# Optimization experiments

Measured on AMD Instinct MI355X. Metric: run time of the kernel, lower is better.

## Reference

```python
import jax, jax.numpy as jnp
import numpy as np

B_, L_, DM, DI, N, R, K = 2, 1024, 1024, 2048, 16, 64, 4
EPS = 1e-5

def silu(x):
    return x * jax.nn.sigmoid(x)

def causal_conv1d(x, w, b):
    # x: (B,L,D); w: (D,K) depthwise. torch Conv1d(padding=K-1) then slice [:L] == left-pad causal conv.
    L = x.shape[1]
    xp = jnp.pad(x, ((0, 0), (K - 1, 0), (0, 0)))
    y = xp[:, 0:L, :] * w[:, 0]
    for k in range(1, K):
        y = y + xp[:, k:k + L, :] * w[:, k]
    return y + b

def selective_scan(u, delta, A, Bm, Cm, D):
    # u, delta: (B,L,D); A: (D,N); Bm, Cm: (B,L,N)
    dA = jnp.exp(jnp.einsum('bld,dn->bldn', delta, A))
    dBu = jnp.einsum('bld,bln,bld->bldn', delta, Bm, u)
    h0 = jnp.zeros((u.shape[0], u.shape[2], A.shape[1]), u.dtype)
    def step(h, xs):
        dA_t, dBu_t, C_t = xs
        h = dA_t * h + dBu_t
        return h, jnp.einsum('bdn,bn->bd', h, C_t)
    _, ys = jax.lax.scan(step, h0, (jnp.moveaxis(dA, 1, 0), jnp.moveaxis(dBu, 1, 0), jnp.moveaxis(Cm, 1, 0)))
    return jnp.moveaxis(ys, 0, 1) + u * D  # (B,L,D)

def branch(x, conv_w, conv_b, Wx, Wdt, bdt, A_log, D):
    x = silu(causal_conv1d(x, conv_w, conv_b))
    dbl = x @ Wx.T                               # (B,L,R+2N)
    dt, Bm, Cm = dbl[..., :R], dbl[..., R:R + N], dbl[..., R + N:]
    dt = dt @ Wdt.T + bdt                        # dt_proj is Linear WITH bias in source
    delta = jax.nn.softplus(dt + bdt)            # source also passes delta_bias to the scan (bias added twice; faithful)
    A = -jnp.exp(A_log)
    return selective_scan(x, delta, A, Bm, Cm, D)

def reference(a, b, Wi, conv_w, conv_b, Wx, Wdt, bdt, A_log, D,
              conv_w_b, conv_b_b, Wx_b, Wdt_b, bdt_b, A_log_b, D_b, Wo, norm_w):
    xz_a = a @ Wi.T
    x_f, z = xz_a[..., :DI], xz_a[..., DI:]
    y_f = branch(x_f, conv_w, conv_b, Wx, Wdt, bdt, A_log, D)
    xz_b = jnp.flip(b, 1) @ Wi.T
    x_bwd = xz_b[..., :DI]
    y_b = jnp.flip(branch(x_bwd, conv_w_b, conv_b_b, Wx_b, Wdt_b, bdt_b, A_log_b, D_b), 1)
    y = y_f + y_b
    # RMSNormGated, norm_before_gate=False: gate first, then RMSNorm
    g = y * silu(z)
    g = g * jax.lax.rsqrt(jnp.mean(g * g, axis=-1, keepdims=True) + EPS) * norm_w
    return g @ Wo.T

def setup_inputs() -> dict:
    key = jax.random.key(0)
    ks = jax.random.split(key, 16)
    s = 0.02
    def rn(k, shape):
        return jax.random.normal(k, shape, jnp.float32) * s
    def inv_dt(k):
        dt = jnp.exp(jax.random.uniform(k, (DI,)) * (np.log(0.1) - np.log(0.001)) + np.log(0.001))
        dt = jnp.clip(dt, 1e-4, None)
        return dt + jnp.log(-jnp.expm1(-dt))
    A_log = jnp.log(jnp.broadcast_to(jnp.arange(1, N + 1, dtype=jnp.float32), (DI, N)))
    return dict(
        a=jax.random.normal(ks[0], (B_, L_, DM), jnp.float32),
        b=jax.random.normal(ks[1], (B_, L_, DM), jnp.float32),
        Wi=rn(ks[2], (2 * DI, DM)),
        conv_w=rn(ks[3], (DI, K)), conv_b=rn(ks[4], (DI,)),
        Wx=rn(ks[5], (R + 2 * N, DI)), Wdt=rn(ks[6], (DI, R)), bdt=inv_dt(ks[7]),
        A_log=A_log, D=jnp.ones((DI,), jnp.float32),
        conv_w_b=rn(ks[8], (DI, K)), conv_b_b=rn(ks[9], (DI,)),
        Wx_b=rn(ks[10], (R + 2 * N, DI)), Wdt_b=rn(ks[11], (DI, R)), bdt_b=inv_dt(ks[12]),
        A_log_b=A_log, D_b=jnp.ones((DI,), jnp.float32),
        Wo=rn(ks[13], (DM, DI)), norm_w=jnp.ones((DI,), jnp.float32),
    )
```

## Files before the change

### kernel.cpp

```cpp
#include <hip/hip_runtime.h>
#include <hip/hip_bf16.h>
#include <cmath>

#define B_ 2
#define L_ 1024
#define DM 1024
#define DI 2048
#define NS 16
#define RR 64
#define KC 4
#define NCH 64
#define CL (L_ / NCH)
#define NSPLIT 16

using frag8 = __attribute__((ext_vector_type(8))) short;
using facc4 = __attribute__((ext_vector_type(4))) float;
using f32x4 = __attribute__((ext_vector_type(4))) float;

struct alignas(8) S4v { short x, y, z, w; };

__device__ __forceinline__ short f2b(float v) {
    __hip_bfloat16 h = __float2bfloat16(v);
    return *(short*)&h;
}

__device__ __forceinline__ float silu1(float x) {
    return x / (1.f + __expf(-x));
}

__device__ __forceinline__ int swz(int r, int q) {
    return (r * 4 + (q ^ (r & 3))) ^ (((r >> 2) & 1) << 2);
}
__device__ __forceinline__ void swz_src(int l, int& R, int& C) {
    int rho = l >> 2;
    R = rho ^ ((rho >> 2) & 1);
    C = (l & 3) ^ (R & 3);
}

__device__ __forceinline__ void pow4(float qv, f32x4& p0, f32x4& p1, f32x4& p2, f32x4& p3) {
    float q2 = qv * qv, q3 = q2 * qv, q4 = q2 * q2;
    p0 = (f32x4){qv, q2, q3, q4};
    f32x4 s4 = {q4, q4, q4, q4};
    p1 = p0 * s4;
    f32x4 s8 = s4 * s4;
    p2 = p0 * s8;
    p3 = p1 * s8;
}

__device__ __forceinline__ void async_ld16(const void* g, void* l) {
    __builtin_amdgcn_global_load_lds(
        (const __attribute__((address_space(1))) unsigned int*)g,
        (__attribute__((address_space(3))) unsigned int*)l, 16, 0, 0);
}

__device__ __forceinline__ void cvt4(const float* __restrict__ src, size_t si,
                                     short* __restrict__ dst, size_t di2) {
    float4 v = *(const float4*)(src + si);
    S4v r = { f2b(v.x), f2b(v.y), f2b(v.z), f2b(v.w) };
    *(S4v*)(dst + di2) = r;
}

__global__ void cvt_all(const float* __restrict__ a, const float* __restrict__ b,
                        const float* __restrict__ Wi,
                        const float* __restrict__ Wx, const float* __restrict__ Wxb2,
                        const float* __restrict__ Wdt, const float* __restrict__ Wdtb2,
                        const float* __restrict__ Wo,
                        short* __restrict__ abf, short* __restrict__ bbf,
                        short* __restrict__ Wibf,
                        short* __restrict__ Wxbf, short* __restrict__ Wxbbf,
                        short* __restrict__ Wdtbf, short* __restrict__ Wdtbbf,
                        short* __restrict__ Wobf) {
    size_t i = ((size_t)blockIdx.x * 256 + threadIdx.x) * 4;
    const size_t S_ab = (size_t)B_ * L_ * DM;
    if (i < S_ab) { cvt4(a, i, abf, i); return; } i -= S_ab;
    if (i < S_ab) {
        size_t r = i / DM, c = i % DM;
        size_t bb = r / L_, ll = r % L_;
        size_t sr = bb * L_ + (L_ - 1 - ll);
        cvt4(b, sr * DM + c, bbf, i); return;
    } i -= S_ab;
    const size_t S_wi = (size_t)2 * DI * DM;
    if (i < S_wi) { cvt4(Wi, i, Wibf, i); return; } i -= S_wi;
    const size_t S_wx = (size_t)96 * DI;
    if (i < S_wx) { cvt4(Wx, i, Wxbf, i); return; } i -= S_wx;
    if (i < S_wx) { cvt4(Wxb2, i, Wxbbf, i); return; } i -= S_wx;
    const size_t S_wd = (size_t)DI * RR;
    if (i < S_wd) { cvt4(Wdt, i, Wdtbf, i); return; } i -= S_wd;
    if (i < S_wd) { cvt4(Wdtb2, i, Wdtbbf, i); return; } i -= S_wd;
    const size_t S_wo = (size_t)DM * DI;
    if (i < S_wo) cvt4(Wo, i, Wobf, i);
}

template <int BM>
__device__ __forceinline__ void gemm_body(
    const short* A, int lda, const short* W, int ldw, int wRowOff,
    float* C, int ldc, int K, int m0, int n0) {
    constexpr int MF = BM / 32;
    __shared__ __align__(16) short As[2][BM * 32];
    __shared__ __align__(16) short Ws[2][64 * 32];
    const int tid = threadIdx.x;
    const int lane = tid & 63, wv = tid >> 6;
    const int wm = (wv & 1) * (BM / 2), wn = (wv >> 1) * 32;
    const int q = lane >> 4, mr = lane & 15;
    int sR, sC; swz_src(lane, sR, sC);
    const int sg = swz(mr, q) * 8;

    const short* Ag = A + (size_t)(m0 + wv * 16 + sR) * lda + sC * 8;
    const short* Wg = W + (size_t)(n0 + wRowOff + wv * 16 + sR) * ldw + sC * 8;

    facc4 acc[MF][2];
#pragma unroll
    for (int i = 0; i < MF; ++i)
#pragma unroll
        for (int j = 0; j < 2; ++j) acc[i][j] = (facc4){0.f, 0.f, 0.f, 0.f};

    async_ld16(Ag, &As[0][wv * 512]);
    if constexpr (BM == 128) async_ld16(Ag + (size_t)64 * lda, &As[0][wv * 512 + 2048]);
    async_ld16(Wg, &Ws[0][wv * 512]);

    const int nk = K / 32;
    for (int it = 0; it < nk; ++it) {
        const int buf = it & 1;
        __syncthreads();
        if (it + 1 < nk) {
            int k0 = (it + 1) * 32;
            async_ld16(Ag + k0, &As[buf ^ 1][wv * 512]);
            if constexpr (BM == 128)
                async_ld16(Ag + (size_t)64 * lda + k0, &As[buf ^ 1][wv * 512 + 2048]);
            async_ld16(Wg + k0, &Ws[buf ^ 1][wv * 512]);
        }
        frag8 af[MF], wf[2];
#pragma unroll
        for (int t = 0; t < MF; ++t)
            af[t] = *(const frag8*)&As[buf][(wm + t * 16) * 32 + sg];
#pragma unroll
        for (int j = 0; j < 2; ++j)
            wf[j] = *(const frag8*)&Ws[buf][(wn + j * 16) * 32 + sg];
#pragma unroll
        for (int i = 0; i < MF; ++i)
#pragma unroll
            for (int j = 0; j < 2; ++j)
                acc[i][j] = __builtin_amdgcn_mfma_f32_16x16x32_bf16(af[i], wf[j], acc[i][j], 0, 0, 0);
    }
#pragma unroll
    for (int i = 0; i < MF; ++i)
#pragma unroll
        for (int j = 0; j < 2; ++j) {
            int gn = n0 + wn + j * 16 + mr;
#pragma unroll
            for (int e = 0; e < 4; ++e) {
                int gm = m0 + wm + i * 16 + q * 4 + e;
                C[(size_t)gm * ldc + gn] = acc[i][j][e];
            }
        }
}

__global__ __launch_bounds__(256) void gemm_xz_conv(
    const short* __restrict__ abf, const short* __restrict__ bbf,
    const short* __restrict__ Wibf,
    float* __restrict__ UF, float* __restrict__ UB, float* __restrict__ Z,
    short* __restrict__ CFo, short* __restrict__ CBo,
    const float* __restrict__ cwf, const float* __restrict__ cbf2,
    const float* __restrict__ cwb, const float* __restrict__ cbb2) {
    __shared__ __align__(16) char smem[26624];
    short (*As)[4608] = (short (*)[4608])smem;
    short (*Ws)[2048] = (short (*)[2048])(smem + 18432);
    float (*Xs)[68] = (float (*)[68])smem;

    const int bz = blockIdx.z;
    const bool isX = (bz != 2);
    const int tid = threadIdx.x;
    const int lane = tid & 63, wv = tid >> 6;
    {
    }
    const int id = blockIdx.y * gridDim.x + blockIdx.x;
    const int xcd = id & 7, idx = id >> 3;
    const int nt = (xcd & 3) * 8 + (idx & 7);
    const int mt = (xcd >> 2) * 8 + (idx >> 3);
    const int m0 = mt * 128, n0 = nt * 64;
    const bool hasHalo = isX && (m0 % L_ != 0);
    const int wm = (wv & 1) * 64, wn = (wv >> 1) * 32;
    const int q = lane >> 4, mr = lane & 15;
    int sR, sC; swz_src(lane, sR, sC);
    const int sg = swz(mr, q) * 8;

    const short* A = (bz == 1) ? bbf : abf;
    const int wOff = (bz == 2) ? DI : 0;

    const short* Ag  = A + (size_t)(m0 + wv * 16 + sR) * DM + sC * 8;
    const short* Agh = A + (size_t)(m0 - 16 + sR) * DM + sC * 8;
    const short* Wg  = Wibf + (size_t)(n0 + wOff + wv * 16 + sR) * DM + sC * 8;

    facc4 acc[4][2], hacc[2];
#pragma unroll
    for (int i = 0; i < 4; ++i)
#pragma unroll
        for (int j = 0; j < 2; ++j) acc[i][j] = (facc4){0.f, 0.f, 0.f, 0.f};
#pragma unroll
    for (int j = 0; j < 2; ++j) hacc[j] = (facc4){0.f, 0.f, 0.f, 0.f};

    async_ld16(Ag, &As[0][wv * 512]);
    async_ld16(Ag + (size_t)64 * DM, &As[0][wv * 512 + 2048]);
    async_ld16(Wg, &Ws[0][wv * 512]);
    if (hasHalo && wv == 0) async_ld16(Agh, &As[0][4096]);

    const int nk = DM / 32;
    for (int it = 0; it < nk; ++it) {
        const int buf = it & 1;
        __syncthreads();
        if (it + 1 < nk) {
            int k0 = (it + 1) * 32;
            async_ld16(Ag + k0, &As[buf ^ 1][wv * 512]);
            async_ld16(Ag + (size_t)64 * DM + k0, &As[buf ^ 1][wv * 512 + 2048]);
            async_ld16(Wg + k0, &Ws[buf ^ 1][wv * 512]);
            if (hasHalo && wv == 0) async_ld16(Agh + k0, &As[buf ^ 1][4096]);
        }
        frag8 af[4], wf[2];
#pragma unroll
        for (int t = 0; t < 4; ++t)
            af[t] = *(const frag8*)&As[buf][(wm + t * 16) * 32 + sg];
#pragma unroll
        for (int j = 0; j < 2; ++j)
            wf[j] = *(const frag8*)&Ws[buf][(wn + j * 16) * 32 + sg];
        if (hasHalo && wm == 0) {
            frag8 afh = *(const frag8*)&As[buf][4096 + sg];
#pragma unroll
            for (int j = 0; j < 2; ++j)
                hacc[j] = __builtin_amdgcn_mfma_f32_16x16x32_bf16(afh, wf[j], hacc[j], 0, 0, 0);
        }
#pragma unroll
        for (int i = 0; i < 4; ++i)
#pragma unroll
            for (int j = 0; j < 2; ++j)
                acc[i][j] = __builtin_amdgcn_mfma_f32_16x16x32_bf16(af[i], wf[j], acc[i][j], 0, 0, 0);
    }

    if (!isX) {
#pragma unroll
        for (int i = 0; i < 4; ++i)
#pragma unroll
            for (int j = 0; j < 2; ++j) {
                int gn = n0 + wn + j * 16 + mr;
#pragma unroll
                for (int e = 0; e < 4; ++e) {
                    int gm = m0 + wm + i * 16 + q * 4 + e;
                    Z[(size_t)gm * DI + gn] = acc[i][j][e];
                }
            }
        return;
    }

    const float* cw = (bz == 1) ? cwb : cwf;
    const float* cb = (bz == 1) ? cbb2 : cbf2;
    float* U   = (bz == 1) ? UB : UF;
    short* Co  = (bz == 1) ? CBo : CFo;
    const int col = tid & 63;
    const int dcol = n0 + col;
    const int rg = tid >> 6;
    float4 wd = *(const float4*)(cw + (size_t)dcol * KC);
    float bd = cb[dcol];

    __syncthreads();
#pragma unroll
    for (int p = 0; p < 2; ++p) {
        if (p == 0) {
            if ((wv & 1) == 0) {
#pragma unroll
                for (int j = 0; j < 2; ++j) {
#pragma unroll
                    for (int e = 0; e < 4; ++e)
                        Xs[q * 4 + e][wn + j * 16 + mr] = hacc[j][e];
#pragma unroll
                    for (int i = 0; i < 4; ++i)
#pragma unroll
                        for (int e = 0; e < 4; ++e)
                            Xs[16 + i * 16 + q * 4 + e][wn + j * 16 + mr] = acc[i][j][e];
                }
            }
        } else {
            if ((wv & 1) == 0) {
#pragma unroll
                for (int j = 0; j < 2; ++j)
#pragma unroll
                    for (int e = 0; e < 4; ++e)
                        Xs[q * 4 + e][wn + j * 16 + mr] = acc[3][j][e];
            } else {
#pragma unroll
                for (int j = 0; j < 2; ++j)
#pragma unroll
                    for (int i = 0; i < 4; ++i)
#pragma unroll
                        for (int e = 0; e < 4; ++e)
                            Xs[16 + i * 16 + q * 4 + e][wn + j * 16 + mr] = acc[i][j][e];
            }
        }
        __syncthreads();
#pragma unroll
        for (int rr = 0; rr < 16; ++rr) {
            int rl = rg * 16 + rr;
            float x0 = Xs[13 + rl][col];
            float x1 = Xs[14 + rl][col];
            float x2 = Xs[15 + rl][col];
            float x3 = Xs[16 + rl][col];
            float v = bd + x0 * wd.x + x1 * wd.y + x2 * wd.z + x3 * wd.w;
            float s2 = silu1(v);
            size_t go = (size_t)(m0 + p * 64 + rl) * DI + dcol;
            U[go] = s2;
            Co[go] = f2b(s2);
        }
        if (p == 0) __syncthreads();
    }
}

__global__ __launch_bounds__(256) void gemm_dt(
    const short* __restrict__ dtf, const short* __restrict__ dtb,
    const short* __restrict__ Wf, const short* __restrict__ Wb,
    float* __restrict__ DTF_, float* __restrict__ DTB_) {
    const int bz = blockIdx.z;
    gemm_body<64>(bz ? dtb : dtf, RR, bz ? Wb : Wf, RR, 0,
                  bz ? DTB_ : DTF_, DI, RR, blockIdx.y * 64, blockIdx.x * 64);
}

__global__ __launch_bounds__(256) void gemm_out(
    const short* __restrict__ gbf, const short* __restrict__ Wobf,
    float* __restrict__ out) {
    gemm_body<64>(gbf, DI, Wobf, DI, 0, out, DM, DI, blockIdx.y * 64, blockIdx.x * 64);
}

__global__ __launch_bounds__(256) void gemm_dbl(
    const short* __restrict__ CF, const short* __restrict__ CB,
    const short* __restrict__ Wxf, const short* __restrict__ Wxb,
    float* __restrict__ part) {
    __shared__ __align__(16) short As[2][128 * 32];
    __shared__ __align__(16) short Ws[2][96 * 32];
    const int br = blockIdx.z / NSPLIT, zz = blockIdx.z % NSPLIT;
    const short* A = br ? CB : CF;
    const short* W = br ? Wxb : Wxf;
    constexpr int Kchunk = DI / NSPLIT;
    const int tid = threadIdx.x;
    const int lane = tid & 63, wv = tid >> 6;
    const int m0 = blockIdx.y * 128;
    const int kOff = zz * Kchunk;
    const int wm = (wv & 1) * 64, wn = (wv >> 1) * 48;
    const int q = lane >> 4, mr = lane & 15;
    int sR, sC; swz_src(lane, sR, sC);
    const int sg = swz(mr, q) * 8;

    const short* Ag = A + (size_t)(m0 + wv * 16 + sR) * DI + sC * 8 + kOff;
    const short* Wg = W + (size_t)(wv * 16 + sR) * DI + sC * 8 + kOff;

    facc4 acc[4][3];
#pragma unroll
    for (int i = 0; i < 4; ++i)
#pragma unroll
        for (int j = 0; j < 3; ++j) acc[i][j] = (facc4){0.f, 0.f, 0.f, 0.f};

    async_ld16(Ag, &As[0][wv * 512]);
    async_ld16(Ag + (size_t)64 * DI, &As[0][wv * 512 + 2048]);
    async_ld16(Wg, &Ws[0][wv * 512]);
    if (wv < 2) async_ld16(Wg + (size_t)64 * DI, &Ws[0][wv * 512 + 2048]);

    const int nk = Kchunk / 32;
    for (int it = 0; it < nk; ++it) {
        const int buf = it & 1;
        __syncthreads();
        if (it + 1 < nk) {
            int k0 = (it + 1) * 32;
            async_ld16(Ag + k0, &As[buf ^ 1][wv * 512]);
            async_ld16(Ag + (size_t)64 * DI + k0, &As[buf ^ 1][wv * 512 + 2048]);
            async_ld16(Wg + k0, &Ws[buf ^ 1][wv * 512]);
            if (wv < 2) async_ld16(Wg + (size_t)64 * DI + k0, &Ws[buf ^ 1][wv * 512 + 2048]);
        }
        frag8 af[4], wf[3];
#pragma unroll
        for (int t = 0; t < 4; ++t)
            af[t] = *(const frag8*)&As[buf][(wm + t * 16) * 32 + sg];
#pragma unroll
        for (int j = 0; j < 3; ++j)
            wf[j] = *(const frag8*)&Ws[buf][(wn + j * 16) * 32 + sg];
#pragma unroll
        for (int i = 0; i < 4; ++i)
#pragma unroll
            for (int j = 0; j < 3; ++j)
                acc[i][j] = __builtin_amdgcn_mfma_f32_16x16x32_bf16(af[i], wf[j], acc[i][j], 0, 0, 0);
    }
    float* Cz = part + (size_t)blockIdx.z * (B_ * L_) * 96;
#pragma unroll
    for (int i = 0; i < 4; ++i)
#pragma unroll
        for (int j = 0; j < 3; ++j) {
            int gn = wn + j * 16 + mr;
#pragma unroll
            for (int e = 0; e < 4; ++e) {
                int gm = m0 + wm + i * 16 + q * 4 + e;
                Cz[(size_t)gm * 96 + gn] = acc[i][j][e];
            }
        }
}

__global__ void reduce_dbl(const float* __restrict__ part,
                           float* __restrict__ dblf, float* __restrict__ dblb,
                           short* __restrict__ dtf, short* __restrict__ dtb) {
    int idx = blockIdx.x * blockDim.x + threadIdx.x;
    const int T = B_ * L_ * 96;
    int br = 0;
    if (idx >= T) { br = 1; idx -= T; }
    const float* p = part + (size_t)br * NSPLIT * T;
    float s = 0.f;
#pragma unroll
    for (int z = 0; z < NSPLIT; ++z) s += p[(size_t)z * T + idx];
    (br ? dblb : dblf)[idx] = s;
    int row = idx / 96, col = idx % 96;
    if (col < RR) (br ? dtb : dtf)[(size_t)row * RR + col] = f2b(s);
}

__device__ __forceinline__ float softplus2(float raw, float bd2) {
    float x = raw + bd2;
    return (x > 20.f) ? x : log1pf(__expf(x));
}

__global__ void scan_chunk(float* UF, float* UB, float* DTFm, float* DTBm,
                           const float* bdtf, const float* bdtb,
                           const float* dblF, const float* dblB,
                           const float* Alf, const float* Alb,
                           const float* Dvf, const float* Dvb,
                           float* PF, float* SF, float* PB, float* SB) {
    __shared__ __align__(16) float BCs[CL][32];
    const int tid = threadIdx.x;
    const int d = blockIdx.x * 256 + tid;
    const int br = blockIdx.y >> 1, bb = blockIdx.y & 1;
    const int c = blockIdx.z;
    const int l0 = c * CL;
    float* __restrict__ u = br ? UB : UF;
    float* __restrict__ dtm = br ? DTBm : DTFm;
    const float* __restrict__ bdt = br ? bdtb : bdtf;
    const float* __restrict__ dbl = br ? dblB : dblF;
    const float* __restrict__ A_log = br ? Alb : Alf;
    const float* __restrict__ Dv = br ? Dvb : Dvf;
    float* __restrict__ Pbuf = br ? PB : PF;
    float* __restrict__ Sbuf = br ? SB : SF;
    {
        int e = tid * 2;
        int row = e >> 5, cc = e & 31;
        *(float2*)&BCs[row][cc] =
            *(const float2*)(dbl + ((size_t)(bb * L_ + l0 + row) * 96 + 64 + cc));
    }
    float Av[NS];
#pragma unroll
    for (int n = 0; n < NS; ++n) Av[n] = -__expf(A_log[d * NS + n]);
    bool structured = true;
#pragma unroll
    for (int n = 1; n < NS; ++n)
        structured = structured &&
            (fabsf(Av[n] - (n + 1) * Av[0]) <= 1e-4f * (n + 1) * fabsf(Av[0]));
    const float bd2 = 2.f * bdt[d];
    const float Dd = Dv[d];
    float cd = 0.f;
    __syncthreads();
    float* __restrict__ up = u + ((size_t)bb * L_ + l0) * DI + d;
    float* __restrict__ dp = dtm + ((size_t)bb * L_ + l0) * DI + d;
    size_t pb = ((size_t)(bb * NCH + c) * NS) * DI + d;

    if (structured) {
        const float Av0 = Av[0];
        f32x4 S4[4];
#pragma unroll
        for (int m = 0; m < 4; ++m) S4[m] = (f32x4){0.f, 0.f, 0.f, 0.f};
        float draw = dp[0], ul = up[0];
        for (int l = 0; l < CL; ++l) {
            float draw_n = 0.f, ul_n = 0.f;
            if (l + 1 < CL) { draw_n = dp[(size_t)(l + 1) * DI]; ul_n = up[(size_t)(l + 1) * DI]; }
            float x = draw + bd2;
            float e = __expf(x);
            float del = (x > 20.f) ? x : __logf(1.f + e);
            cd += del;
            float du = del * ul;
            f32x4 pw0, pw1, pw2, pw3;
            pow4(__expf(del * Av0), pw0, pw1, pw2, pw3);
            const f32x4* BC4 = (const f32x4*)&BCs[l][0];
            f32x4 b0 = BC4[0], b1 = BC4[1], b2 = BC4[2], b3 = BC4[3];
            f32x4 c0 = BC4[4], c1 = BC4[5], c2 = BC4[6], c3 = BC4[7];
            f32x4 du4 = {du, du, du, du};
            S4[0] = pw0 * S4[0] + du4 * b0;
            S4[1] = pw1 * S4[1] + du4 * b1;
            S4[2] = pw2 * S4[2] + du4 * b2;
            S4[3] = pw3 * S4[3] + du4 * b3;
            f32x4 pA = S4[0] * c0 + S4[1] * c1;
            f32x4 pB = S4[2] * c2 + S4[3] * c3;
            f32x4 pv = pA + pB;
            float accv = (pv[0] + pv[1]) + (pv[2] + pv[3]);
            dp[(size_t)l * DI] = cd;
            up[(size_t)l * DI] = accv + ul * Dd;
            draw = draw_n; ul = ul_n;
        }
        f32x4 pw0, pw1, pw2, pw3;
        pow4(__expf(cd * Av0), pw0, pw1, pw2, pw3);
        f32x4 pws[4] = {pw0, pw1, pw2, pw3};
#pragma unroll
        for (int m = 0; m < 4; ++m)
#pragma unroll
            for (int k2 = 0; k2 < 4; ++k2) {
                Pbuf[pb + (size_t)(m * 4 + k2) * DI] = pws[m][k2];
                Sbuf[pb + (size_t)(m * 4 + k2) * DI] = S4[m][k2];
            }
    } else {
        float S[NS];
#pragma unroll
        for (int n = 0; n < NS; ++n) S[n] = 0.f;
        float draw = dp[0], ul = up[0];
        for (int l = 0; l < CL; ++l) {
            float draw_n = 0.f, ul_n = 0.f;
            if (l + 1 < CL) { draw_n = dp[(size_t)(l + 1) * DI]; ul_n = up[(size_t)(l + 1) * DI]; }
            float del = softplus2(draw, bd2);
            cd += del;
            float du = del * ul;
            const float* Brow = &BCs[l][0];
            float pa[4] = {0.f, 0.f, 0.f, 0.f};
#pragma unroll
            for (int j = 0; j < 4; ++j)
#pragma unroll
                for (int k = 0; k < 4; ++k) {
                    int n = j * 4 + k;
                    float dA = __expf(del * Av[n]);
                    S[n] = fmaf(dA, S[n], du * Brow[n]);
                    pa[j] = fmaf(S[n], Brow[16 + n], pa[j]);
                }
            float accv = (pa[0] + pa[1]) + (pa[2] + pa[3]);
            dp[(size_t)l * DI] = cd;
            up[(size_t)l * DI] = accv + ul * Dd;
            draw = draw_n; ul = ul_n;
        }
#pragma unroll
        for (int n = 0; n < NS; ++n) {
            Pbuf[pb + (size_t)n * DI] = __expf(cd * Av[n]);
            Sbuf[pb + (size_t)n * DI] = S[n];
        }
    }
}

__global__ void scan_combine(float* __restrict__ PF, const float* __restrict__ SF,
                             float* __restrict__ PB, const float* __restrict__ SB) {
    int g = blockIdx.x * blockDim.x + threadIdx.x;
    const int T = B_ * NS * DI;
    float* __restrict__ P = (g < T) ? PF : PB;
    const float* __restrict__ S = (g < T) ? SF : SB;
    int gg = (g < T) ? g : g - T;
    int d = gg % DI;
    int rest = gg / DI;
    int n = rest % NS, bb = rest / NS;
    const size_t stride = (size_t)NS * DI;
    size_t o = ((size_t)(bb * NCH) * NS + n) * DI + d;
    float h = 0.f;
    float Pc[4], Sc[4], Pn[4], Sn[4];
#pragma unroll
    for (int i = 0; i < 4; ++i) { Pc[i] = P[o + (size_t)i * stride]; Sc[i] = S[o + (size_t)i * stride]; }
    for (int c = 0; c < NCH; c += 4) {
        if (c + 4 < NCH) {
#pragma unroll
            for (int i = 0; i < 4; ++i) {
                Pn[i] = P[o + (size_t)(i + 4) * stride];
                Sn[i] = S[o + (size_t)(i + 4) * stride];
            }
        }
#pragma unroll
        for (int i = 0; i < 4; ++i) {
            P[o] = h;
            h = fmaf(Pc[i], h, Sc[i]);
            o += stride;
        }
#pragma unroll
        for (int i = 0; i < 4; ++i) { Pc[i] = Pn[i]; Sc[i] = Sn[i]; }
    }
}

__global__ void scan_apply(float* UF, float* UB,
                           const float* DTFm, const float* DTBm,
                           const float* dblF, const float* dblB,
                           const float* Alf, const float* Alb,
                           const float* PF, const float* PB) {
    __shared__ __align__(16) float Cs[CL][16];
    const int tid = threadIdx.x;
    const int d = blockIdx.x * 256 + tid;
    const int br = blockIdx.y >> 1, bb = blockIdx.y & 1;
    const int c = blockIdx.z + 1;
    const int l0 = c * CL;
    float* __restrict__ y = br ? UB : UF;
    const float* __restrict__ cdm = br ? DTBm : DTFm;
    const float* __restrict__ dbl = br ? dblB : dblF;
    const float* __restrict__ A_log = br ? Alb : Alf;
    const float* __restrict__ Hbuf = br ? PB : PF;
    {
        int row = tid >> 4, cc = tid & 15;
        Cs[row][cc] = dbl[(size_t)(bb * L_ + l0 + row) * 96 + 80 + cc];
    }
    float Av[NS];
#pragma unroll
    for (int n = 0; n < NS; ++n) Av[n] = -__expf(A_log[d * NS + n]);
    bool structured = true;
#pragma unroll
    for (int n = 1; n < NS; ++n)
        structured = structured &&
            (fabsf(Av[n] - (n + 1) * Av[0]) <= 1e-4f * (n + 1) * fabsf(Av[0]));
    size_t pb = ((size_t)(bb * NCH + c) * NS) * DI + d;
    const float* __restrict__ cp = cdm + ((size_t)bb * L_ + l0) * DI + d;
    float* __restrict__ yp = y + ((size_t)bb * L_ + l0) * DI + d;

    if (structured) {
        f32x4 ch4[4];
#pragma unroll
        for (int m = 0; m < 4; ++m)
#pragma unroll
            for (int k2 = 0; k2 < 4; ++k2)
                ch4[m][k2] = Hbuf[pb + (size_t)(m * 4 + k2) * DI];
        __syncthreads();
        const float Av0 = Av[0];
        float cdv = cp[0], yv = yp[0];
        for (int l = 0; l < CL; ++l) {
            float cdn = 0.f, yn = 0.f;
            if (l + 1 < CL) { cdn = cp[(size_t)(l + 1) * DI]; yn = yp[(size_t)(l + 1) * DI]; }
            f32x4 pw0, pw1, pw2, pw3;
            pow4(__expf(cdv * Av0), pw0, pw1, pw2, pw3);
            const f32x4* C4 = (const f32x4*)&Cs[l][0];
            f32x4 pA = pw0 * (C4[0] * ch4[0]) + pw1 * (C4[1] * ch4[1]);
            f32x4 pB = pw2 * (C4[2] * ch4[2]) + pw3 * (C4[3] * ch4[3]);
            f32x4 pv = pA + pB;
            yp[(size_t)l * DI] = yv + (pv[0] + pv[1]) + (pv[2] + pv[3]);
            cdv = cdn; yv = yn;
        }
    } else {
        float chs[NS];
#pragma unroll
        for (int n = 0; n < NS; ++n) chs[n] = Hbuf[pb + (size_t)n * DI];
        __syncthreads();
        float cdv = cp[0], yv = yp[0];
        for (int l = 0; l < CL; ++l) {
            float cdn = 0.f, yn = 0.f;
            if (l + 1 < CL) { cdn = cp[(size_t)(l + 1) * DI]; yn = yp[(size_t)(l + 1) * DI]; }
            const float* Crow = &Cs[l][0];
            float pa[4] = {0.f, 0.f, 0.f, 0.f};
#pragma unroll
            for (int j = 0; j < 4; ++j)
#pragma unroll
                for (int k = 0; k < 4; ++k) {
                    int n = j * 4 + k;
                    pa[j] = fmaf(__expf(cdv * Av[n]), Crow[n] * chs[n], pa[j]);
                }
            yp[(size_t)l * DI] = yv + (pa[0] + pa[1]) + (pa[2] + pa[3]);
            cdv = cdn; yv = yn;
        }
    }
}

__global__ void combine_rms(const float* __restrict__ yf, const float* __restrict__ yb,
                            const float* __restrict__ z,
                            const float* __restrict__ nw,
                            short* __restrict__ g) {
    int row = blockIdx.x;
    int bb = row / L_, l = row % L_;
    int tid = threadIdx.x;
    size_t base = (size_t)row * DI;
    size_t baseb = ((size_t)bb * L_ + (L_ - 1 - l)) * DI;
    float4 gv[2];
    float ss = 0.f;
#pragma unroll
    for (int j = 0; j < 2; ++j) {
        int d = tid * 4 + j * 1024;
        float4 a4 = *(const float4*)(yf + base + d);
        float4 b4 = *(const float4*)(yb + baseb + d);
        float4 z4 = *(const float4*)(z + base + d);
        float4 r;
        r.x = (a4.x + b4.x) * silu1(z4.x);
        r.y = (a4.y + b4.y) * silu1(z4.y);
        r.z = (a4.z + b4.z) * silu1(z4.z);
        r.w = (a4.w + b4.w) * silu1(z4.w);
        gv[j] = r;
        ss += r.x * r.x + r.y * r.y + r.z * r.z + r.w * r.w;
    }
#pragma unroll
    for (int off = 32; off > 0; off >>= 1) ss += __shfl_down(ss, off, 64);
    __shared__ float red[4];
    if ((tid & 63) == 0) red[tid >> 6] = ss;
    __syncthreads();
    float tot = red[0] + red[1] + red[2] + red[3];
    float rms = rsqrtf(tot / (float)DI + 1e-5f);
#pragma unroll
    for (int j = 0; j < 2; ++j) {
        int d = tid * 4 + j * 1024;
        float4 w4 = *(const float4*)(nw + d);
        S4v o = { f2b(gv[j].x * rms * w4.x), f2b(gv[j].y * rms * w4.y),
                  f2b(gv[j].z * rms * w4.z), f2b(gv[j].w * rms * w4.w) };
        *(S4v*)(g + base + d) = o;
    }
}

extern "C" void kernel_launch(void* const* d_in, const int* in_sizes, int n_in,
                              void* d_out, int out_size, void* d_ws, size_t ws_size,
                              hipStream_t stream) {
    const float* a      = (const float*)d_in[0];
    const float* b      = (const float*)d_in[1];
    const float* Wi     = (const float*)d_in[2];
    const float* conv_w = (const float*)d_in[3];
    const float* conv_b = (const float*)d_in[4];
    const float* Wx     = (const float*)d_in[5];
    const float* Wdt    = (const float*)d_in[6];
    const float* bdt    = (const float*)d_in[7];
    const float* A_log  = (const float*)d_in[8];
    const float* Dvec   = (const float*)d_in[9];
    const float* conv_w_b = (const float*)d_in[10];
    const float* conv_b_b = (const float*)d_in[11];
    const float* Wx_b   = (const float*)d_in[12];
    const float* Wdt_b  = (const float*)d_in[13];
    const float* bdt_b  = (const float*)d_in[14];
    const float* A_log_b = (const float*)d_in[15];
    const float* Dvec_b = (const float*)d_in[16];
    const float* Wo     = (const float*)d_in[17];
    const float* nw     = (const float*)d_in[18];
    float* out = (float*)d_out;

    const int M = B_ * L_;
    const size_t BLD = (size_t)M * DI;
    const size_t NDBL = (size_t)M * 96;
    const size_t PSsz = (size_t)NCH * B_ * NS * DI;

    float* f = (float*)d_ws;
    float* Zb   = f;  f += BLD;
    float* UF   = f;  f += BLD;
    float* UB   = f;  f += BLD;
    float* DTF  = f;  f += BLD;
    float* DTB  = f;  f += BLD;
    float* dblf = f;  f += NDBL;
    float* dblb = f;  f += NDBL;
    float* Pf   = f;  f += PSsz;
    float* Sf   = f;  f += PSsz;
    float* Pb   = f;  f += PSsz;
    float* Sb   = f;  f += PSsz;
    float* part = Pf;

    short* s = (short*)f;
    short* abf    = s;  s += (size_t)M * DM;
    short* bbf    = s;  s += (size_t)M * DM;
    short* Wibf   = s;  s += (size_t)2 * DI * DM;
    short* CF     = s;  s += BLD;
    short* CB     = s;  s += BLD;
    short* Wxbf   = s;  s += (size_t)96 * DI;
    short* Wxbbf  = s;  s += (size_t)96 * DI;
    short* Wdtbf  = s;  s += (size_t)DI * RR;
    short* Wdtbbf = s;  s += (size_t)DI * RR;
    short* dtfbf  = s;  s += (size_t)M * RR;
    short* dtbbf  = s;  s += (size_t)M * RR;
    short* Wobf   = s;  s += (size_t)DM * DI;
    short* gbf    = abf;

    dim3 blk(256);

    cvt_all<<<dim3(10880), blk, 0, stream>>>(a, b, Wi, Wx, Wx_b, Wdt, Wdt_b, Wo,
                                             abf, bbf, Wibf, Wxbf, Wxbbf, Wdtbf, Wdtbbf, Wobf);
    gemm_xz_conv<<<dim3(DI / 64, M / 128, 3), blk, 0, stream>>>(
        abf, bbf, Wibf, UF, UB, Zb, CF, CB,
        conv_w, conv_b, conv_w_b, conv_b_b);
    gemm_dbl<<<dim3(1, M / 128, 2 * NSPLIT), blk, 0, stream>>>(CF, CB, Wxbf, Wxbbf, part);
    reduce_dbl<<<dim3(2 * (int)(NDBL / 256)), blk, 0, stream>>>(part, dblf, dblb, dtfbf, dtbbf);
    gemm_dt<<<dim3(DI / 64, M / 64, 2), blk, 0, stream>>>(dtfbf, dtbbf, Wdtbf, Wdtbbf, DTF, DTB);
    scan_chunk<<<dim3(DI / 256, 4, NCH), blk, 0, stream>>>(
        UF, UB, DTF, DTB, bdt, bdt_b, dblf, dblb, A_log, A_log_b, Dvec, Dvec_b,
        Pf, Sf, Pb, Sb);
    scan_combine<<<dim3(2 * B_ * NS * DI / 256), blk, 0, stream>>>(Pf, Sf, Pb, Sb);
    scan_apply<<<dim3(DI / 256, 4, NCH - 1), blk, 0, stream>>>(
        UF, UB, DTF, DTB, dblf, dblb, A_log, A_log_b, Pf, Pb);
    combine_rms<<<dim3(M), blk, 0, stream>>>(UF, UB, Zb, nw, gbf);
    gemm_out<<<dim3(DM / 64, M / 64), blk, 0, stream>>>(gbf, Wobf, out);
}
```

Measured before the change: 294.8 us.

## Fuse x and z input projections per block and recompute chunk decay in combine

```diff
diff --git a/kernel.cpp b/kernel.cpp
--- a/kernel.cpp
+++ b/kernel.cpp
@@ -11,7 +11,7 @@
 #define KC 4
 #define NCH 64
 #define CL (L_ / NCH)
-#define NSPLIT 16
+#define NSPLIT 8
 
 using frag8 = __attribute__((ext_vector_type(8))) short;
 using facc4 = __attribute__((ext_vector_type(4))) float;
@@ -162,46 +162,49 @@
     short* __restrict__ CFo, short* __restrict__ CBo,
     const float* __restrict__ cwf, const float* __restrict__ cbf2,
     const float* __restrict__ cwb, const float* __restrict__ cbb2) {
-    __shared__ __align__(16) char smem[26624];
-    short (*As)[4608] = (short (*)[4608])smem;
-    short (*Ws)[2048] = (short (*)[2048])(smem + 18432);
+    __shared__ __align__(16) char smem[34816];
+    short (*As)[4608]  = (short (*)[4608])smem;
+    short (*Wsx)[2048] = (short (*)[2048])(smem + 18432);
+    short (*Wsz)[2048] = (short (*)[2048])(smem + 26624);
     float (*Xs)[68] = (float (*)[68])smem;
 
     const int bz = blockIdx.z;
-    const bool isX = (bz != 2);
+    const bool hasZ = (bz == 0);
     const int tid = threadIdx.x;
     const int lane = tid & 63, wv = tid >> 6;
-    {
-    }
     const int id = blockIdx.y * gridDim.x + blockIdx.x;
     const int xcd = id & 7, idx = id >> 3;
     const int nt = (xcd & 3) * 8 + (idx & 7);
     const int mt = (xcd >> 2) * 8 + (idx >> 3);
     const int m0 = mt * 128, n0 = nt * 64;
-    const bool hasHalo = isX && (m0 % L_ != 0);
+    const bool hasHalo = (m0 % L_ != 0);
     const int wm = (wv & 1) * 64, wn = (wv >> 1) * 32;
     const int q = lane >> 4, mr = lane & 15;
     int sR, sC; swz_src(lane, sR, sC);
     const int sg = swz(mr, q) * 8;
 
-    const short* A = (bz == 1) ? bbf : abf;
-    const int wOff = (bz == 2) ? DI : 0;
+    const short* A = bz ? bbf : abf;
 
     const short* Ag  = A + (size_t)(m0 + wv * 16 + sR) * DM + sC * 8;
     const short* Agh = A + (size_t)(m0 - 16 + sR) * DM + sC * 8;
-    const short* Wg  = Wibf + (size_t)(n0 + wOff + wv * 16 + sR) * DM + sC * 8;
-
-    facc4 acc[4][2], hacc[2];
+    const short* Wgx = Wibf + (size_t)(n0 + wv * 16 + sR) * DM + sC * 8;
+    const short* Wgz = Wibf + (size_t)(n0 + DI + wv * 16 + sR) * DM + sC * 8;
+
+    facc4 accx[4][2], accz[4][2], hacc[2];
 #pragma unroll
     for (int i = 0; i < 4; ++i)
 #pragma unroll
-        for (int j = 0; j < 2; ++j) acc[i][j] = (facc4){0.f, 0.f, 0.f, 0.f};
+        for (int j = 0; j < 2; ++j) {
+            accx[i][j] = (facc4){0.f, 0.f, 0.f, 0.f};
+            accz[i][j] = (facc4){0.f, 0.f, 0.f, 0.f};
+        }
 #pragma unroll
     for (int j = 0; j < 2; ++j) hacc[j] = (facc4){0.f, 0.f, 0.f, 0.f};
 
     async_ld16(Ag, &As[0][wv * 512]);
     async_ld16(Ag + (size_t)64 * DM, &As[0][wv * 512 + 2048]);
-    async_ld16(Wg, &Ws[0][wv * 512]);
+    async_ld16(Wgx, &Wsx[0][wv * 512]);
+    if (hasZ) async_ld16(Wgz, &Wsz[0][wv * 512]);
     if (hasHalo && wv == 0) async_ld16(Agh, &As[0][4096]);
 
     const int nk = DM / 32;
@@ -212,30 +215,43 @@
             int k0 = (it + 1) * 32;
             async_ld16(Ag + k0, &As[buf ^ 1][wv * 512]);
             async_ld16(Ag + (size_t)64 * DM + k0, &As[buf ^ 1][wv * 512 + 2048]);
-            async_ld16(Wg + k0, &Ws[buf ^ 1][wv * 512]);
+            async_ld16(Wgx + k0, &Wsx[buf ^ 1][wv * 512]);
+            if (hasZ) async_ld16(Wgz + k0, &Wsz[buf ^ 1][wv * 512]);
             if (hasHalo && wv == 0) async_ld16(Agh + k0, &As[buf ^ 1][4096]);
         }
-        frag8 af[4], wf[2];
+        frag8 af[4], wfx[2], wfz[2];
 #pragma unroll
         for (int t = 0; t < 4; ++t)
             af[t] = *(const frag8*)&As[buf][(wm + t * 16) * 32 + sg];
 #pragma unroll
         for (int j = 0; j < 2; ++j)
-            wf[j] = *(const frag8*)&Ws[buf][(wn + j * 16) * 32 + sg];
+            wfx[j] = *(const frag8*)&Wsx[buf][(wn + j * 16) * 32 + sg];
+        if (hasZ) {
+#pragma unroll
+            for (int j = 0; j < 2; ++j)
+                wfz[j] = *(const frag8*)&Wsz[buf][(wn + j * 16) * 32 + sg];
+        }
         if (hasHalo && wm == 0) {
             frag8 afh = *(const frag8*)&As[buf][4096 + sg];
 #pragma unroll
             for (int j = 0; j < 2; ++j)
-                hacc[j] = __builtin_amdgcn_mfma_f32_16x16x32_bf16(afh, wf[j], hacc[j], 0, 0, 0);
+                hacc[j] = __builtin_amdgcn_mfma_f32_16x16x32_bf16(afh, wfx[j], hacc[j], 0, 0, 0);
         }
 #pragma unroll
         for (int i = 0; i < 4; ++i)
 #pragma unroll
             for (int j = 0; j < 2; ++j)
-                acc[i][j] = __builtin_amdgcn_mfma_f32_16x16x32_bf16(af[i], wf[j], acc[i][j], 0, 0, 0);
-    }
-
-    if (!isX) {
+                accx[i][j] = __builtin_amdgcn_mfma_f32_16x16x32_bf16(af[i], wfx[j], accx[i][j], 0, 0, 0);
+        if (hasZ) {
+#pragma unroll
+            for (int i = 0; i < 4; ++i)
+#pragma unroll
+                for (int j = 0; j < 2; ++j)
+                    accz[i][j] = __builtin_amdgcn_mfma_f32_16x16x32_bf16(af[i], wfz[j], accz[i][j], 0, 0, 0);
+        }
+    }
+
+    if (hasZ) {
 #pragma unroll
         for (int i = 0; i < 4; ++i)
 #pragma unroll
@@ -244,16 +260,15 @@
 #pragma unroll
                 for (int e = 0; e < 4; ++e) {
                     int gm = m0 + wm + i * 16 + q * 4 + e;
-                    Z[(size_t)gm * DI + gn] = acc[i][j][e];
+                    Z[(size_t)gm * DI + gn] = accz[i][j][e];
                 }
             }
-        return;
-    }
-
-    const float* cw = (bz == 1) ? cwb : cwf;
-    const float* cb = (bz == 1) ? cbb2 : cbf2;
-    float* U   = (bz == 1) ? UB : UF;
-    short* Co  = (bz == 1) ? CBo : CFo;
+    }
+
+    const float* cw = bz ? cwb : cwf;
+    const float* cb = bz ? cbb2 : cbf2;
+    float* U   = bz ? UB : UF;
+    short* Co  = bz ? CBo : CFo;
     const int col = tid & 63;
     const int dcol = n0 + col;
     const int rg = tid >> 6;
@@ -274,7 +289,7 @@
                     for (int i = 0; i < 4; ++i)
 #pragma unroll
                         for (int e = 0; e < 4; ++e)
-                            Xs[16 + i * 16 + q * 4 + e][wn + j * 16 + mr] = acc[i][j][e];
+                            Xs[16 + i * 16 + q * 4 + e][wn + j * 16 + mr] = accx[i][j][e];
                 }
             }
         } else {
@@ -283,7 +298,7 @@
                 for (int j = 0; j < 2; ++j)
 #pragma unroll
                     for (int e = 0; e < 4; ++e)
-                        Xs[q * 4 + e][wn + j * 16 + mr] = acc[3][j][e];
+                        Xs[q * 4 + e][wn + j * 16 + mr] = accx[3][j][e];
             } else {
 #pragma unroll
                 for (int j = 0; j < 2; ++j)
@@ -291,7 +306,7 @@
                     for (int i = 0; i < 4; ++i)
 #pragma unroll
                         for (int e = 0; e < 4; ++e)
-                            Xs[16 + i * 16 + q * 4 + e][wn + j * 16 + mr] = acc[i][j][e];
+                            Xs[16 + i * 16 + q * 4 + e][wn + j * 16 + mr] = accx[i][j][e];
             }
         }
         __syncthreads();
@@ -317,8 +332,8 @@
     const short* __restrict__ Wf, const short* __restrict__ Wb,
     float* __restrict__ DTF_, float* __restrict__ DTB_) {
     const int bz = blockIdx.z;
-    gemm_body<64>(bz ? dtb : dtf, RR, bz ? Wb : Wf, RR, 0,
-                  bz ? DTB_ : DTF_, DI, RR, blockIdx.y * 64, blockIdx.x * 64);
+    gemm_body<128>(bz ? dtb : dtf, RR, bz ? Wb : Wf, RR, 0,
+                   bz ? DTB_ : DTF_, DI, RR, blockIdx.y * 128, blockIdx.x * 64);
 }
 
 __global__ __launch_bounds__(256) void gemm_out(
@@ -424,7 +439,7 @@
                            const float* dblF, const float* dblB,
                            const float* Alf, const float* Alb,
                            const float* Dvf, const float* Dvb,
-                           float* PF, float* SF, float* PB, float* SB) {
+                           float* SF, float* SB) {
     __shared__ __align__(16) float BCs[CL][32];
     const int tid = threadIdx.x;
     const int d = blockIdx.x * 256 + tid;
@@ -437,7 +452,6 @@
     const float* __restrict__ dbl = br ? dblB : dblF;
     const float* __restrict__ A_log = br ? Alb : Alf;
     const float* __restrict__ Dv = br ? Dvb : Dvf;
-    float* __restrict__ Pbuf = br ? PB : PF;
     float* __restrict__ Sbuf = br ? SB : SF;
     {
         int e = tid * 2;
@@ -493,16 +507,11 @@
             up[(size_t)l * DI] = accv + ul * Dd;
             draw = draw_n; ul = ul_n;
         }
-        f32x4 pw0, pw1, pw2, pw3;
-        pow4(__expf(cd * Av0), pw0, pw1, pw2, pw3);
-        f32x4 pws[4] = {pw0, pw1, pw2, pw3};
 #pragma unroll
         for (int m = 0; m < 4; ++m)
 #pragma unroll
-            for (int k2 = 0; k2 < 4; ++k2) {
-                Pbuf[pb + (size_t)(m * 4 + k2) * DI] = pws[m][k2];
+            for (int k2 = 0; k2 < 4; ++k2)
                 Sbuf[pb + (size_t)(m * 4 + k2) * DI] = S4[m][k2];
-            }
     } else {
         float S[NS];
 #pragma unroll
@@ -531,45 +540,54 @@
             draw = draw_n; ul = ul_n;
         }
 #pragma unroll
-        for (int n = 0; n < NS; ++n) {
-            Pbuf[pb + (size_t)n * DI] = __expf(cd * Av[n]);
+        for (int n = 0; n < NS; ++n)
             Sbuf[pb + (size_t)n * DI] = S[n];
-        }
     }
 }
 
 __global__ void scan_combine(float* __restrict__ PF, const float* __restrict__ SF,
-                             float* __restrict__ PB, const float* __restrict__ SB) {
+                             float* __restrict__ PB, const float* __restrict__ SB,
+                             const float* __restrict__ DTFm, const float* __restrict__ DTBm,
+                             const float* __restrict__ Alf, const float* __restrict__ Alb) {
     int g = blockIdx.x * blockDim.x + threadIdx.x;
     const int T = B_ * NS * DI;
-    float* __restrict__ P = (g < T) ? PF : PB;
-    const float* __restrict__ S = (g < T) ? SF : SB;
-    int gg = (g < T) ? g : g - T;
+    int br = (g >= T);
+    int gg = br ? g - T : g;
+    float* __restrict__ P = br ? PB : PF;
+    const float* __restrict__ S = br ? SB : SF;
+    const float* __restrict__ cdm = br ? DTBm : DTFm;
+    const float* __restrict__ Alog = br ? Alb : Alf;
     int d = gg % DI;
     int rest = gg / DI;
     int n = rest % NS, bb = rest / NS;
+    const float Avn = -__expf(Alog[d * NS + n]);
     const size_t stride = (size_t)NS * DI;
+    const size_t cstride = (size_t)CL * DI;
     size_t o = ((size_t)(bb * NCH) * NS + n) * DI + d;
+    const float* cp = cdm + ((size_t)bb * L_ + CL - 1) * DI + d;
     float h = 0.f;
-    float Pc[4], Sc[4], Pn[4], Sn[4];
-#pragma unroll
-    for (int i = 0; i < 4; ++i) { Pc[i] = P[o + (size_t)i * stride]; Sc[i] = S[o + (size_t)i * stride]; }
+    float Cc[4], Sc[4], Cn[4], Sn[4];
+#pragma unroll
+    for (int i = 0; i < 4; ++i) {
+        Cc[i] = cp[(size_t)i * cstride];
+        Sc[i] = S[o + (size_t)i * stride];
+    }
     for (int c = 0; c < NCH; c += 4) {
         if (c + 4 < NCH) {
 #pragma unroll
             for (int i = 0; i < 4; ++i) {
-                Pn[i] = P[o + (size_t)(i + 4) * stride];
+                Cn[i] = cp[(size_t)(c + i + 4) * cstride];
                 Sn[i] = S[o + (size_t)(i + 4) * stride];
             }
         }
 #pragma unroll
         for (int i = 0; i < 4; ++i) {
             P[o] = h;
-            h = fmaf(Pc[i], h, Sc[i]);
+            h = fmaf(__expf(Cc[i] * Avn), h, Sc[i]);
             o += stride;
         }
 #pragma unroll
-        for (int i = 0; i < 4; ++i) { Pc[i] = Pn[i]; Sc[i] = Sn[i]; }
+        for (int i = 0; i < 4; ++i) { Cc[i] = Cn[i]; Sc[i] = Sn[i]; }
     }
 }
 
@@ -755,16 +773,17 @@
 
     cvt_all<<<dim3(10880), blk, 0, stream>>>(a, b, Wi, Wx, Wx_b, Wdt, Wdt_b, Wo,
                                              abf, bbf, Wibf, Wxbf, Wxbbf, Wdtbf, Wdtbbf, Wobf);
-    gemm_xz_conv<<<dim3(DI / 64, M / 128, 3), blk, 0, stream>>>(
+    gemm_xz_conv<<<dim3(DI / 64, M / 128, 2), blk, 0, stream>>>(
         abf, bbf, Wibf, UF, UB, Zb, CF, CB,
         conv_w, conv_b, conv_w_b, conv_b_b);
     gemm_dbl<<<dim3(1, M / 128, 2 * NSPLIT), blk, 0, stream>>>(CF, CB, Wxbf, Wxbbf, part);
     reduce_dbl<<<dim3(2 * (int)(NDBL / 256)), blk, 0, stream>>>(part, dblf, dblb, dtfbf, dtbbf);
-    gemm_dt<<<dim3(DI / 64, M / 64, 2), blk, 0, stream>>>(dtfbf, dtbbf, Wdtbf, Wdtbbf, DTF, DTB);
+    gemm_dt<<<dim3(DI / 64, M / 128, 2), blk, 0, stream>>>(dtfbf, dtbbf, Wdtbf, Wdtbbf, DTF, DTB);
     scan_chunk<<<dim3(DI / 256, 4, NCH), blk, 0, stream>>>(
         UF, UB, DTF, DTB, bdt, bdt_b, dblf, dblb, A_log, A_log_b, Dvec, Dvec_b,
-        Pf, Sf, Pb, Sb);
-    scan_combine<<<dim3(2 * B_ * NS * DI / 256), blk, 0, stream>>>(Pf, Sf, Pb, Sb);
+        Sf, Sb);
+    scan_combine<<<dim3(2 * B_ * NS * DI / 256), blk, 0, stream>>>(
+        Pf, Sf, Pb, Sb, DTF, DTB, A_log, A_log_b);
     scan_apply<<<dim3(DI / 256, 4, NCH - 1), blk, 0, stream>>>(
         UF, UB, DTF, DTB, dblf, dblb, A_log, A_log_b, Pf, Pb);
     combine_rms<<<dim3(M), blk, 0, stream>>>(UF, UB, Zb, nw, gbf);
```

Result: faster. 288.5 us (-2.1%).
